# Kernel tuning notes

Measured on AMD Instinct MI355X. Metric: run time of the kernel, lower is better.

Reference implementation:

```python
import jax, jax.numpy as jnp
import numpy as np

NUM_HEADS = 8
NUM_GROUPS = 32
EMB = 512
EPS = 1e-5


def setup_inputs() -> dict:
    key = jax.random.key(0)
    ks = jax.random.split(key, 12)
    B, C, H, W = 256, EMB, 16, 16
    s = 1.0 / np.sqrt(C)
    x = jax.random.normal(ks[0], (B, C, H, W), dtype=jnp.float32)
    Wq = jax.random.normal(ks[1], (C, EMB), dtype=jnp.float32) * s
    bq = jax.random.normal(ks[2], (EMB,), dtype=jnp.float32) * 0.01
    Wk = jax.random.normal(ks[3], (C, EMB), dtype=jnp.float32) * s
    bk = jax.random.normal(ks[4], (EMB,), dtype=jnp.float32) * 0.01
    Wv = jax.random.normal(ks[5], (C, EMB), dtype=jnp.float32) * s
    bv = jax.random.normal(ks[6], (EMB,), dtype=jnp.float32) * 0.01
    Wf = jax.random.normal(ks[7], (EMB, EMB), dtype=jnp.float32) * s
    bf = jax.random.normal(ks[8], (EMB,), dtype=jnp.float32) * 0.01
    gn_w = jnp.ones((EMB,), dtype=jnp.float32)
    gn_b = jnp.zeros((EMB,), dtype=jnp.float32)
    return {"x": x, "Wq": Wq, "bq": bq, "Wk": Wk, "bk": bk,
            "Wv": Wv, "bv": bv, "Wf": Wf, "bf": bf,
            "gn_w": gn_w, "gn_b": gn_b}


def reference(x, Wq, bq, Wk, bk, Wv, bv, Wf, bf, gn_w, gn_b):
    B, C, H, W = x.shape
    S = H * W
    nh = NUM_HEADS
    dh = EMB // nh
    xs = x.reshape(B, C, S).transpose(0, 2, 1)  # [B, S, C]
    q = (xs @ Wq + bq).reshape(B, S, nh, dh)
    k = (xs @ Wk + bk).reshape(B, S, nh, dh)
    v = (xs @ Wv + bv).reshape(B, S, nh, dh)
    scale = dh ** -0.5
    logits = jnp.einsum('bshd,bthd->bhst', q, k) * scale  # [B, nh, S, S]
    attn = jax.nn.softmax(logits, axis=-1)
    o = jnp.einsum('bhst,bthd->bshd', attn, v).reshape(B, S, EMB)
    o = o @ Wf + bf  # [B, S, EMB]
    y = o.transpose(0, 2, 1).reshape(B, EMB, H, W) + x  # residual
    # GroupNorm over (channels-within-group, H, W)
    G = NUM_GROUPS
    yg = y.reshape(B, G, EMB // G, H, W)
    mu = jnp.mean(yg, axis=(2, 3, 4), keepdims=True)
    var = jnp.var(yg, axis=(2, 3, 4), keepdims=True)
    yn = ((yg - mu) * jax.lax.rsqrt(var + EPS)).reshape(B, EMB, H, W)
    return yn * gn_w.reshape(1, EMB, 1, 1) + gn_b.reshape(1, EMB, 1, 1)
```

## Files before the change

kernel.cpp:

```cpp
#include <hip/hip_runtime.h>
#include <hip/hip_bf16.h>
#include <stdint.h>

#define B_  256
#define C_  512
#define S_  256
#define NH  8
#define DH  64

typedef float f32x4 __attribute__((ext_vector_type(4)));
typedef short s16x8 __attribute__((ext_vector_type(8)));

static __device__ __forceinline__ unsigned short f2bf(float f) {
  union { float f; unsigned u; } v; v.f = f;
  unsigned r = v.u + 0x7FFFu + ((v.u >> 16) & 1u);
  return (unsigned short)(r >> 16);
}

static __device__ __forceinline__ unsigned pk_bf16(float lo, float hi) {
  unsigned r;
  asm("v_cvt_pk_bf16_f32 %0, %1, %2" : "=v"(r) : "v"(lo), "v"(hi));
  return r;
}

static __device__ __forceinline__ void gload_lds16(const void* g, void* l) {
  __builtin_amdgcn_global_load_lds((const __attribute__((address_space(1))) void*)g,
                                   (__attribute__((address_space(3))) void*)l,
                                   16, 0, 0);
}

__global__ __launch_bounds__(256) void prep_w(const float* __restrict__ Wq,
                                              const float* __restrict__ Wk,
                                              const float* __restrict__ Wv,
                                              const float* __restrict__ Wf,
                                              unsigned short* __restrict__ Wqkvt,
                                              unsigned short* __restrict__ Wft) {
  int mat = blockIdx.z;
  const float* src = (mat == 0) ? Wq : (mat == 1) ? Wk : (mat == 2) ? Wv : Wf;
  unsigned short* dst = (mat < 3) ? (Wqkvt + (size_t)mat * 512 * 512) : Wft;
  int n0 = blockIdx.x * 64, c0 = blockIdx.y * 64;
  __shared__ float tile[64][65];
  int t = threadIdx.x;
  int tr = t >> 4;
  int tc = (t & 15) * 4;
#pragma unroll
  for (int i = 0; i < 4; ++i) {
    int c = tr + i * 16;
    float4 v = *(const float4*)&src[(size_t)(c0 + c) * 512 + n0 + tc];
    tile[c][tc + 0] = v.x; tile[c][tc + 1] = v.y;
    tile[c][tc + 2] = v.z; tile[c][tc + 3] = v.w;
  }
  __syncthreads();
#pragma unroll
  for (int i = 0; i < 4; ++i) {
    int n = tr + i * 16;
    ushort4 o;
    o.x = f2bf(tile[tc + 0][n]); o.y = f2bf(tile[tc + 1][n]);
    o.z = f2bf(tile[tc + 2][n]); o.w = f2bf(tile[tc + 3][n]);
    *(ushort4*)&dst[(size_t)(n0 + n) * 512 + c0 + tc] = o;
  }
}

__global__ __launch_bounds__(256) void prep_x(const float* __restrict__ x,
                                              unsigned short* __restrict__ xs) {
  int b = blockIdx.z, s0 = blockIdx.x * 64, c0 = blockIdx.y * 64;
  __shared__ float tile[64][65];
  int t = threadIdx.x;
  int tr = t >> 4, tc = (t & 15) * 4;
  const float* xb = x + (size_t)b * C_ * S_;
#pragma unroll
  for (int i = 0; i < 4; ++i) {
    int c = tr + i * 16;
    float4 v = *(const float4*)&xb[(size_t)(c0 + c) * S_ + s0 + tc];
    tile[c][tc + 0] = v.x; tile[c][tc + 1] = v.y;
    tile[c][tc + 2] = v.z; tile[c][tc + 3] = v.w;
  }
  __syncthreads();
  unsigned short* xsb = xs + (size_t)b * S_ * C_;
#pragma unroll
  for (int i = 0; i < 4; ++i) {
    int s = tr + i * 16;
    ushort4 o;
    o.x = f2bf(tile[tc + 0][s]); o.y = f2bf(tile[tc + 1][s]);
    o.z = f2bf(tile[tc + 2][s]); o.w = f2bf(tile[tc + 3][s]);
    *(ushort4*)&xsb[(size_t)(s0 + s) * C_ + c0 + tc] = o;
  }
}

__global__ __launch_bounds__(256) void qkv_gemm(const unsigned short* __restrict__ xs,
                                                const unsigned short* __restrict__ Wqkvt,
                                                const float* __restrict__ bq,
                                                const float* __restrict__ bk,
                                                const float* __restrict__ bv,
                                                unsigned short* __restrict__ qout,
                                                unsigned short* __restrict__ kout,
                                                unsigned short* __restrict__ vout) {
  __shared__ char lds[32768];
  int bid = blockIdx.x;
  int lin = (bid & 7) * 768 + (bid >> 3);
  int b = lin / 24, r24 = lin % 24;
  int mt = r24 / 12, nt = r24 % 12;
  int t = threadIdx.x, lane = t & 63, w = t >> 6;
  int l15 = lane & 15, l4 = lane >> 4;
  int wr = w >> 1, wc = w & 1;
  const unsigned short* xsb = xs + ((size_t)b * S_ + mt * 128) * C_;
  const unsigned short* wt  = Wqkvt + (size_t)nt * 128 * C_;

#define QSTAGE(kt, p)                                                         \
  {                                                                           \
    _Pragma("unroll")                                                         \
    for (int i = 0; i < 2; ++i) {                                             \
      int ch = i * 256 + t, r = ch >> 2, g = ch & 3;                          \
      int gs = g ^ ((r ^ (r >> 2)) & 3);                                      \
      gload_lds16(xsb + (size_t)r * C_ + (kt) * 32 + gs * 8,                  \
                  lds + (p) * 16384 + ch * 16);                               \
    }                                                                         \
    _Pragma("unroll")                                                         \
    for (int i = 0; i < 2; ++i) {                                             \
      int ch = i * 256 + t, r = ch >> 2, g = ch & 3;                          \
      int gs = g ^ ((r ^ (r >> 2)) & 3);                                      \
      gload_lds16(wt + (size_t)r * C_ + (kt) * 32 + gs * 8,                   \
                  lds + (p) * 16384 + 8192 + ch * 16);                        \
    }                                                                         \
  }

  f32x4 acc[4][4] = {};
  QSTAGE(0, 0);
  __syncthreads();

  for (int kt = 0; kt < 16; ++kt) {
    if (kt < 15) QSTAGE(kt + 1, (kt + 1) & 1);
    const char* Ab = lds + (kt & 1) * 16384;
    const char* Bb = Ab + 8192;
    s16x8 af[4], bfr[4];
#pragma unroll
    for (int fi = 0; fi < 4; ++fi) {
      int r = wr * 64 + fi * 16 + l15;
      af[fi] = *(const s16x8*)(Ab + r * 64 + ((l4 ^ ((r ^ (r >> 2)) & 3)) << 4));
    }
#pragma unroll
    for (int fj = 0; fj < 4; ++fj) {
      int r = wc * 64 + fj * 16 + l15;
      bfr[fj] = *(const s16x8*)(Bb + r * 64 + ((l4 ^ ((r ^ (r >> 2)) & 3)) << 4));
    }
#pragma unroll
    for (int fi = 0; fi < 4; ++fi)
#pragma unroll
      for (int fj = 0; fj < 4; ++fj)
        acc[fi][fj] = __builtin_amdgcn_mfma_f32_16x16x32_bf16(af[fi], bfr[fj], acc[fi][fj], 0, 0, 0);
    __syncthreads();
  }
#undef QSTAGE

  int s_base = mt * 128 + wr * 64;
#pragma unroll
  for (int fj = 0; fj < 4; ++fj) {
    int n_glob = nt * 128 + wc * 64 + fj * 16;
    int sel = n_glob >> 9;
    int within = n_glob & 511;
    int h = within >> 6, dbase = within & 63;
    const float* bias = (sel == 0) ? bq : (sel == 1) ? bk : bv;
    float bias_v = bias[within + l15];
    int d = dbase + l15;
    if (sel == 2) {
      unsigned short* vt = vout + (((size_t)b * NH + h) * DH + d) * (size_t)S_;
#pragma unroll
      for (int fi = 0; fi < 4; ++fi) {
        int srow = s_base + fi * 16 + l4 * 4;
        ushort4 o4;
        o4.x = f2bf(acc[fi][fj][0] + bias_v);
        o4.y = f2bf(acc[fi][fj][1] + bias_v);
        o4.z = f2bf(acc[fi][fj][2] + bias_v);
        o4.w = f2bf(acc[fi][fj][3] + bias_v);
        *(ushort4*)&vt[srow] = o4;
      }
    } else {
      unsigned short* dst = (sel == 0) ? qout : kout;
      unsigned short* dhead = dst + ((size_t)b * NH + h) * S_ * DH;
#pragma unroll
      for (int fi = 0; fi < 4; ++fi) {
        int srow = s_base + fi * 16 + l4 * 4;
#pragma unroll
        for (int rg = 0; rg < 4; ++rg)
          dhead[(size_t)(srow + rg) * DH + d] = f2bf(acc[fi][fj][rg] + bias_v);
      }
    }
  }
}

__global__ __launch_bounds__(512) void attn(const unsigned short* __restrict__ q,
                                            const unsigned short* __restrict__ k,
                                            const unsigned short* __restrict__ vt,
                                            unsigned short* __restrict__ o) {
  int h = blockIdx.x, b = blockIdx.y;
  const unsigned short* qh  = q  + ((size_t)b * NH + h) * S_ * DH;
  const unsigned short* kh  = k  + ((size_t)b * NH + h) * S_ * DH;
  const unsigned short* vth = vt + ((size_t)b * NH + h) * DH * S_;
  __shared__ unsigned short Ks[256 * 72];
  __shared__ unsigned short Vs[64 * 264];
  int t = threadIdx.x, lane = t & 63, w = t >> 6;
  int l15 = lane & 15, l4 = lane >> 4;

  s16x8 qf[2][2];
#pragma unroll
  for (int fi = 0; fi < 2; ++fi)
#pragma unroll
    for (int kk = 0; kk < 2; ++kk) {
      int row = w * 32 + fi * 16 + l15;
      qf[fi][kk] = *(const s16x8*)&qh[(size_t)row * DH + kk * 32 + l4 * 8];
    }

#pragma unroll
  for (int i = 0; i < 4; ++i) {
    int ch = i * 512 + t;
    int r = ch >> 3, g = ch & 7;
    int r64 = r & 63, w32 = r64 & 31;
    int rho = (r & 192) + (r64 >> 5) * 32 + ((w32 >> 2) & 1) * 16 + (w32 >> 3) * 4 + (w32 & 3);
    uint4 kv = *(const uint4*)(kh + (size_t)r * DH + g * 8);
    *(uint4*)((char*)Ks + rho * 144 + g * 16) = kv;
  }
#pragma unroll
  for (int i = 0; i < 4; ++i) {
    int ch = i * 512 + t;
    int d = ch >> 5, c32 = ch & 31;
    uint4 vv = *(const uint4*)(vth + (size_t)d * S_ + c32 * 8);
    *(uint4*)((char*)Vs + d * 528 + c32 * 16) = vv;
  }
  __syncthreads();

  f32x4 acco[4][2] = {};
  float m_run[2] = {-3e38f, -3e38f}, l_run[2] = {0.f, 0.f};
  const float SCL = 0.125f * 1.44269504089f;

  for (int kb = 0; kb < 4; ++kb) {
    f32x4 accs[4][2] = {};
#pragma unroll
    for (int kk = 0; kk < 2; ++kk) {
      s16x8 kf[4];
#pragma unroll
      for (int fj = 0; fj < 4; ++fj)
        kf[fj] = *(const s16x8*)((const char*)Ks + (kb * 64 + fj * 16 + l15) * 144 + kk * 64 + l4 * 16);
#pragma unroll
      for (int fj = 0; fj < 4; ++fj)
#pragma unroll
        for (int fi = 0; fi < 2; ++fi)
          accs[fj][fi] = __builtin_amdgcn_mfma_f32_16x16x32_bf16(kf[fj], qf[fi][kk], accs[fj][fi], 0, 0, 0);
    }
#pragma unroll
    for (int fi = 0; fi < 2; ++fi) {
      float mx = accs[0][fi][0];
#pragma unroll
      for (int fj = 0; fj < 4; ++fj)
#pragma unroll
        for (int rg = 0; rg < 4; ++rg) mx = fmaxf(mx, accs[fj][fi][rg]);
      mx = fmaxf(mx, __shfl_xor(mx, 16, 64));
      mx = fmaxf(mx, __shfl_xor(mx, 32, 64));
      float mnew = fmaxf(m_run[fi], mx);
      float alpha = __builtin_amdgcn_exp2f((m_run[fi] - mnew) * SCL);
      m_run[fi] = mnew;
      float lsum = 0.f;
#pragma unroll
      for (int fj = 0; fj < 4; ++fj)
#pragma unroll
        for (int rg = 0; rg < 4; ++rg) {
          float p = __builtin_amdgcn_exp2f((accs[fj][fi][rg] - mnew) * SCL);
          accs[fj][fi][rg] = p;
          lsum += p;
        }
      lsum += __shfl_xor(lsum, 16, 64);
      lsum += __shfl_xor(lsum, 32, 64);
      l_run[fi] = l_run[fi] * alpha + lsum;
#pragma unroll
      for (int fd = 0; fd < 4; ++fd)
#pragma unroll
        for (int rg = 0; rg < 4; ++rg) acco[fd][fi][rg] *= alpha;
    }
#pragma unroll
    for (int kk2 = 0; kk2 < 2; ++kk2) {
      s16x8 vf[4];
#pragma unroll
      for (int fd = 0; fd < 4; ++fd)
        vf[fd] = *(const s16x8*)((const char*)Vs + (fd * 16 + l15) * 528 + kb * 128 + kk2 * 64 + l4 * 16);
#pragma unroll
      for (int fi = 0; fi < 2; ++fi) {
        union { unsigned u[4]; s16x8 v; } pb;
        pb.u[0] = pk_bf16(accs[2 * kk2][fi][0],     accs[2 * kk2][fi][1]);
        pb.u[1] = pk_bf16(accs[2 * kk2][fi][2],     accs[2 * kk2][fi][3]);
        pb.u[2] = pk_bf16(accs[2 * kk2 + 1][fi][0], accs[2 * kk2 + 1][fi][1]);
        pb.u[3] = pk_bf16(accs[2 * kk2 + 1][fi][2], accs[2 * kk2 + 1][fi][3]);
#pragma unroll
        for (int fd = 0; fd < 4; ++fd)
          acco[fd][fi] = __builtin_amdgcn_mfma_f32_16x16x32_bf16(vf[fd], pb.v, acco[fd][fi], 0, 0, 0);
      }
    }
  }

  unsigned short* ob = o + (size_t)b * S_ * C_ + h * DH;
#pragma unroll
  for (int fi = 0; fi < 2; ++fi) {
    float inv = 1.0f / l_run[fi];
    int qrow = w * 32 + fi * 16 + l15;
#pragma unroll
    for (int fd = 0; fd < 4; ++fd) {
      ushort4 s4;
      s4.x = f2bf(acco[fd][fi][0] * inv);
      s4.y = f2bf(acco[fd][fi][1] * inv);
      s4.z = f2bf(acco[fd][fi][2] * inv);
      s4.w = f2bf(acco[fd][fi][3] * inv);
      *(ushort4*)&ob[(size_t)qrow * C_ + fd * 16 + l4 * 4] = s4;
    }
  }
}

__global__ __launch_bounds__(512) void proj_gn(const unsigned short* __restrict__ o,
                                               const unsigned short* __restrict__ Wft,
                                               const float* __restrict__ bfp,
                                               const float* __restrict__ x,
                                               const float* __restrict__ gnw,
                                               const float* __restrict__ gnb,
                                               float* __restrict__ out) {
  __shared__ char plds[49152];
  __shared__ float red_s[128], red_q[128];
  __shared__ float mu_s[8], rs_s[8];
  int b = blockIdx.y, ct = blockIdx.x;
  int t = threadIdx.x, lane = t & 63, w = t >> 6;
  int l15 = lane & 15, l4 = lane >> 4;
  int wc = w >> 2, wsq = w & 3;
  if (t < 128) { red_s[t] = 0.f; red_q[t] = 0.f; }
  f32x4 acc[4][4] = {};
  const unsigned short* wt = Wft + (size_t)ct * 128 * C_;
  const unsigned short* ob = o + (size_t)b * S_ * C_;

#define PSTAGE(kt, p)                                                         \
  {                                                                           \
    {                                                                         \
      int ch = t, r = ch >> 2, g = ch & 3;                                    \
      int gs = g ^ ((r ^ (r >> 2)) & 3);                                      \
      gload_lds16(wt + (size_t)r * C_ + (kt) * 32 + gs * 8,                   \
                  plds + (p) * 24576 + ch * 16);                              \
    }                                                                         \
    _Pragma("unroll")                                                         \
    for (int i = 0; i < 2; ++i) {                                             \
      int ch = i * 512 + t, r = ch >> 2, g = ch & 3;                          \
      int gs = g ^ ((r ^ (r >> 2)) & 3);                                      \
      gload_lds16(ob + (size_t)r * C_ + (kt) * 32 + gs * 8,                   \
                  plds + (p) * 24576 + 8192 + ch * 16);                       \
    }                                                                         \
  }

  PSTAGE(0, 0);
  __syncthreads();

  for (int kt = 0; kt < 16; ++kt) {
    if (kt < 15) PSTAGE(kt + 1, (kt + 1) & 1);
    const char* Ab = plds + (kt & 1) * 24576;
    const char* Bb = Ab + 8192;
    s16x8 af[4], bfr[4];
#pragma unroll
    for (int fi = 0; fi < 4; ++fi) {
      int r = wc * 64 + fi * 16 + l15;
      af[fi] = *(const s16x8*)(Ab + r * 64 + ((l4 ^ ((r ^ (r >> 2)) & 3)) << 4));
    }
#pragma unroll
    for (int fj = 0; fj < 4; ++fj) {
      int r = wsq * 64 + fj * 16 + l15;
      bfr[fj] = *(const s16x8*)(Bb + r * 64 + ((l4 ^ ((r ^ (r >> 2)) & 3)) << 4));
    }
#pragma unroll
    for (int fi = 0; fi < 4; ++fi)
#pragma unroll
      for (int fj = 0; fj < 4; ++fj)
        acc[fi][fj] = __builtin_amdgcn_mfma_f32_16x16x32_bf16(af[fi], bfr[fj], acc[fi][fj], 0, 0, 0);
    __syncthreads();
  }
#undef PSTAGE

  const float* xb = x + (size_t)b * C_ * S_;
  int c_base = ct * 128 + wc * 64;
  int s_base = wsq * 64;
#pragma unroll
  for (int fi = 0; fi < 4; ++fi)
#pragma unroll
    for (int rg = 0; rg < 4; ++rg) {
      int c = c_base + fi * 16 + l4 * 4 + rg;
      float bias_v = bfp[c];
      float psum = 0.f, psq = 0.f;
#pragma unroll
      for (int fj = 0; fj < 4; ++fj) {
        int s = s_base + fj * 16 + l15;
        float y = acc[fi][fj][rg] + bias_v + xb[(size_t)c * S_ + s];
        acc[fi][fj][rg] = y;
        psum += y; psq += y * y;
      }
#pragma unroll
      for (int off = 1; off < 16; off <<= 1) {
        psum += __shfl_xor(psum, off, 64);
        psq += __shfl_xor(psq, off, 64);
      }
      if (l15 == 0) {
        int cl = c - ct * 128;
        atomicAdd(&red_s[cl], psum);
        atomicAdd(&red_q[cl], psq);
      }
    }
  __syncthreads();
  if (t < 8) {
    float s = 0.f, qq = 0.f;
#pragma unroll
    for (int i = 0; i < 16; ++i) { s += red_s[t * 16 + i]; qq += red_q[t * 16 + i]; }
    float mu = s * (1.0f / 4096.0f);
    float var = qq * (1.0f / 4096.0f) - mu * mu;
    mu_s[t] = mu;
    rs_s[t] = rsqrtf(var + 1e-5f);
  }
  __syncthreads();
  float* outb = out + (size_t)b * C_ * S_;
#pragma unroll
  for (int fi = 0; fi < 4; ++fi)
#pragma unroll
    for (int rg = 0; rg < 4; ++rg) {
      int c = c_base + fi * 16 + l4 * 4 + rg;
      int gl = (c - ct * 128) >> 4;
      float mu = mu_s[gl], rs = rs_s[gl];
      float gw = gnw[c], gb = gnb[c];
#pragma unroll
      for (int fj = 0; fj < 4; ++fj) {
        int s = s_base + fj * 16 + l15;
        outb[(size_t)c * S_ + s] = (acc[fi][fj][rg] - mu) * rs * gw + gb;
      }
    }
}

extern "C" void kernel_launch(void* const* d_in, const int* in_sizes, int n_in,
                              void* d_out, int out_size, void* d_ws, size_t ws_size,
                              hipStream_t stream) {
  const float* x   = (const float*)d_in[0];
  const float* Wq  = (const float*)d_in[1];
  const float* bq  = (const float*)d_in[2];
  const float* Wk  = (const float*)d_in[3];
  const float* bk  = (const float*)d_in[4];
  const float* Wv  = (const float*)d_in[5];
  const float* bv  = (const float*)d_in[6];
  const float* Wf  = (const float*)d_in[7];
  const float* bf  = (const float*)d_in[8];
  const float* gnw = (const float*)d_in[9];
  const float* gnb = (const float*)d_in[10];

  char* ws = (char*)d_ws;
  unsigned short* Wqkvt = (unsigned short*)ws;
  unsigned short* Wft   = (unsigned short*)(ws + 0x180000);
  unsigned short* xs    = (unsigned short*)(ws + 0x200000);
  unsigned short* vbuf  = (unsigned short*)(ws + 0x200000 + (size_t)B_ * S_ * C_ * 2);
  unsigned short* qbuf  = (unsigned short*)d_out;
  unsigned short* kbuf  = qbuf + (size_t)B_ * NH * S_ * DH;
  unsigned short* obuf  = xs;
  float* out = (float*)d_out;

  hipLaunchKernelGGL(prep_w, dim3(8, 8, 4), dim3(256), 0, stream, Wq, Wk, Wv, Wf, Wqkvt, Wft);
  hipLaunchKernelGGL(prep_x, dim3(4, 8, 256), dim3(256), 0, stream, x, xs);
  hipLaunchKernelGGL(qkv_gemm, dim3(6144), dim3(256), 0, stream,
                     xs, Wqkvt, bq, bk, bv, qbuf, kbuf, vbuf);
  hipLaunchKernelGGL(attn, dim3(8, 256), dim3(512), 0, stream, qbuf, kbuf, vbuf, obuf);
  hipLaunchKernelGGL(proj_gn, dim3(4, 256), dim3(512), 0, stream,
                     obuf, Wft, bf, x, gnw, gnb, out);
}
```

Measured before the change: 387.1 us.

## Triple-buffer GEMM LDS staging with vmcnt waits and MFMA priority boosts

The QKV and projection GEMMs move from double to triple buffering in LDS, prefetching two k-tiles ahead. Each iteration now syncs once, using a partial s_waitcnt vmcnt plus a raw barrier instead of two full __syncthreads, so global-to-LDS loads overlap more with MFMA work. s_setprio is raised around MFMA blocks in all three kernels to favour matrix issue. The larger LDS footprint (48KB and 72KB+) may cut occupancy, and the hand-counted vmcnt values must match the number of loads issued per stage.

```diff
diff --git a/kernel.cpp b/kernel.cpp
--- a/kernel.cpp
+++ b/kernel.cpp
@@ -95,7 +95,7 @@
                                                 unsigned short* __restrict__ qout,
                                                 unsigned short* __restrict__ kout,
                                                 unsigned short* __restrict__ vout) {
-  __shared__ char lds[32768];
+  __shared__ char lds[49152];
   int bid = blockIdx.x;
   int lin = (bid & 7) * 768 + (bid >> 3);
   int b = lin / 24, r24 = lin % 24;
@@ -126,11 +126,17 @@
 
   f32x4 acc[4][4] = {};
   QSTAGE(0, 0);
-  __syncthreads();
-
+  QSTAGE(1, 1);
+
+  int cur = 0, stg = 2;
   for (int kt = 0; kt < 16; ++kt) {
-    if (kt < 15) QSTAGE(kt + 1, (kt + 1) & 1);
-    const char* Ab = lds + (kt & 1) * 16384;
+    if (kt < 15) asm volatile("s_waitcnt vmcnt(4)" ::: "memory");
+    else         asm volatile("s_waitcnt vmcnt(0)" ::: "memory");
+    __builtin_amdgcn_s_barrier();
+    asm volatile("" ::: "memory");
+    if (kt + 2 < 16) QSTAGE(kt + 2, stg);
+
+    const char* Ab = lds + cur * 16384;
     const char* Bb = Ab + 8192;
     s16x8 af[4], bfr[4];
 #pragma unroll
@@ -143,12 +149,15 @@
       int r = wc * 64 + fj * 16 + l15;
       bfr[fj] = *(const s16x8*)(Bb + r * 64 + ((l4 ^ ((r ^ (r >> 2)) & 3)) << 4));
     }
+    __builtin_amdgcn_s_setprio(1);
 #pragma unroll
     for (int fi = 0; fi < 4; ++fi)
 #pragma unroll
       for (int fj = 0; fj < 4; ++fj)
         acc[fi][fj] = __builtin_amdgcn_mfma_f32_16x16x32_bf16(af[fi], bfr[fj], acc[fi][fj], 0, 0, 0);
-    __syncthreads();
+    __builtin_amdgcn_s_setprio(0);
+    cur = (cur == 2) ? 0 : cur + 1;
+    stg = (stg == 2) ? 0 : stg + 1;
   }
 #undef QSTAGE
 
@@ -240,11 +249,13 @@
 #pragma unroll
       for (int fj = 0; fj < 4; ++fj)
         kf[fj] = *(const s16x8*)((const char*)Ks + (kb * 64 + fj * 16 + l15) * 144 + kk * 64 + l4 * 16);
+      __builtin_amdgcn_s_setprio(1);
 #pragma unroll
       for (int fj = 0; fj < 4; ++fj)
 #pragma unroll
         for (int fi = 0; fi < 2; ++fi)
           accs[fj][fi] = __builtin_amdgcn_mfma_f32_16x16x32_bf16(kf[fj], qf[fi][kk], accs[fj][fi], 0, 0, 0);
+      __builtin_amdgcn_s_setprio(0);
     }
 #pragma unroll
     for (int fi = 0; fi < 2; ++fi) {
@@ -288,9 +299,11 @@
         pb.u[1] = pk_bf16(accs[2 * kk2][fi][2],     accs[2 * kk2][fi][3]);
         pb.u[2] = pk_bf16(accs[2 * kk2 + 1][fi][0], accs[2 * kk2 + 1][fi][1]);
         pb.u[3] = pk_bf16(accs[2 * kk2 + 1][fi][2], accs[2 * kk2 + 1][fi][3]);
+        __builtin_amdgcn_s_setprio(1);
 #pragma unroll
         for (int fd = 0; fd < 4; ++fd)
           acco[fd][fi] = __builtin_amdgcn_mfma_f32_16x16x32_bf16(vf[fd], pb.v, acco[fd][fi], 0, 0, 0);
+        __builtin_amdgcn_s_setprio(0);
       }
     }
   }
@@ -319,7 +332,7 @@
                                                const float* __restrict__ gnw,
                                                const float* __restrict__ gnb,
                                                float* __restrict__ out) {
-  __shared__ char plds[49152];
+  __shared__ char plds[73728];
   __shared__ float red_s[128], red_q[128];
   __shared__ float mu_s[8], rs_s[8];
   int b = blockIdx.y, ct = blockIdx.x;
@@ -349,11 +362,17 @@
   }
 
   PSTAGE(0, 0);
-  __syncthreads();
-
+  PSTAGE(1, 1);
+
+  int cur = 0, stg = 2;
   for (int kt = 0; kt < 16; ++kt) {
-    if (kt < 15) PSTAGE(kt + 1, (kt + 1) & 1);
-    const char* Ab = plds + (kt & 1) * 24576;
+    if (kt < 15) asm volatile("s_waitcnt vmcnt(3)" ::: "memory");
+    else         asm volatile("s_waitcnt vmcnt(0)" ::: "memory");
+    __builtin_amdgcn_s_barrier();
+    asm volatile("" ::: "memory");
+    if (kt + 2 < 16) PSTAGE(kt + 2, stg);
+
+    const char* Ab = plds + cur * 24576;
     const char* Bb = Ab + 8192;
     s16x8 af[4], bfr[4];
 #pragma unroll
@@ -366,12 +385,15 @@
       int r = wsq * 64 + fj * 16 + l15;
       bfr[fj] = *(const s16x8*)(Bb + r * 64 + ((l4 ^ ((r ^ (r >> 2)) & 3)) << 4));
     }
+    __builtin_amdgcn_s_setprio(1);
 #pragma unroll
     for (int fi = 0; fi < 4; ++fi)
 #pragma unroll
       for (int fj = 0; fj < 4; ++fj)
         acc[fi][fj] = __builtin_amdgcn_mfma_f32_16x16x32_bf16(af[fi], bfr[fj], acc[fi][fj], 0, 0, 0);
-    __syncthreads();
+    __builtin_amdgcn_s_setprio(0);
+    cur = (cur == 2) ? 0 : cur + 1;
+    stg = (stg == 2) ? 0 : stg + 1;
   }
 #undef PSTAGE
 
```

After: 379.9 us. No clear change (-1.9%).
